# Performance work log

Measured on AMD Instinct MI355X. Metric: run time of the kernel, lower is better.

Reference implementation:

```python
import jax, jax.numpy as jnp
import numpy as np

D = 768
H = 8
HD = D // H
FF = 4 * D


def _linear_params(key, din, dout):
    kw, kb = jax.random.split(key)
    lim = 1.0 / np.sqrt(din)
    W = jax.random.uniform(kw, (din, dout), jnp.float32, -lim, lim)
    b = jax.random.uniform(kb, (dout,), jnp.float32, -lim, lim)
    return W, b


def setup_inputs() -> dict:
    key = jax.random.key(0)
    ks = jax.random.split(key, 8)
    x = jax.random.normal(ks[0], (16, 1024, D), jnp.float32)
    Wq, bq = _linear_params(ks[1], D, D)
    Wk, bk = _linear_params(ks[2], D, D)
    Wv, bv = _linear_params(ks[3], D, D)
    Wo, bo = _linear_params(ks[4], D, D)
    W1, b1 = _linear_params(ks[5], D, FF)
    W2, b2 = _linear_params(ks[6], FF, D)
    gamma = jnp.ones((D,), jnp.float32)
    beta = jnp.zeros((D,), jnp.float32)
    return {"x": x, "gamma": gamma, "beta": beta,
            "Wq": Wq, "bq": bq, "Wk": Wk, "bk": bk, "Wv": Wv, "bv": bv,
            "Wo": Wo, "bo": bo, "W1": W1, "b1": b1, "W2": W2, "b2": b2}


def _layernorm(x, gamma, beta, eps=1e-5):
    mu = jnp.mean(x, axis=-1, keepdims=True)
    var = jnp.var(x, axis=-1, keepdims=True)
    return (x - mu) * jax.lax.rsqrt(var + eps) * gamma + beta


def _block(x, gamma, beta, Wq, bq, Wk, bk, Wv, bv, Wo, bo, W1, b1, W2, b2):
    b, n, d = x.shape
    residual = x
    h = _layernorm(x, gamma, beta)
    # QKV projections -> [b, h, n, hd]
    q = (h @ Wq + bq).reshape(b, n, H, HD).transpose(0, 2, 1, 3)
    k = (h @ Wk + bk).reshape(b, n, H, HD).transpose(0, 2, 1, 3)
    v = (h @ Wv + bv).reshape(b, n, H, HD).transpose(0, 2, 1, 3)
    scale = HD ** 0.5
    scores = jnp.einsum('bhid,bhjd->bhij', q, k) / scale
    attn = jax.nn.softmax(scores, axis=-1)
    out = jnp.einsum('bhij,bhjd->bhid', attn, v)
    out = out.transpose(0, 2, 1, 3).reshape(b, n, d)
    out = out @ Wo + bo
    out = out + residual
    residual = out
    h = _layernorm(out, gamma, beta)  # same LN params reused (as in source)
    h = jax.nn.gelu(h @ W1 + b1, approximate=False)
    h = h @ W2 + b2
    return h + residual


def reference(x, gamma, beta, Wq, bq, Wk, bk, Wv, bv, Wo, bo, W1, b1, W2, b2):
    return _block(x, gamma, beta, Wq, bq, Wk, bk, Wv, bv, Wo, bo, W1, b1, W2, b2)
```

## Files before the change

kernel.cpp:

```cpp
#include <hip/hip_runtime.h>

typedef unsigned short u16;
typedef float f32x4 __attribute__((ext_vector_type(4)));
typedef __bf16 bf16x8 __attribute__((ext_vector_type(8)));

#define AS1 __attribute__((address_space(1)))
#define AS3 __attribute__((address_space(3)))

__device__ __forceinline__ float bf2f(u16 h) {
  return __uint_as_float(((unsigned)h) << 16);
}
__device__ __forceinline__ u16 f2bf(float f) {
  unsigned u = __float_as_uint(f);
  unsigned r = (u + 0x7FFFu + ((u >> 16) & 1u)) >> 16;
  return (u16)r;
}
__device__ __forceinline__ void gload16(const u16* g, u16* l) {
  __builtin_amdgcn_global_load_lds((const AS1 void*)g, (AS3 void*)l, 16, 0, 0);
}

__global__ void transpose_k(const float* __restrict__ in, u16* __restrict__ out,
                            int R, int C) {
  __shared__ u16 t[32][33];
  int c0 = blockIdx.x * 32, r0 = blockIdx.y * 32;
  int tx = threadIdx.x & 31, ty = threadIdx.x >> 5;
  for (int i = 0; i < 32; i += 8)
    t[ty + i][tx] = f2bf(in[(size_t)(r0 + ty + i) * C + c0 + tx]);
  __syncthreads();
  for (int i = 0; i < 32; i += 8)
    out[(size_t)(c0 + ty + i) * R + r0 + tx] = t[tx][ty + i];
}

__global__ void transpose4_k(const float* __restrict__ s0, const float* __restrict__ s1,
                             const float* __restrict__ s2, const float* __restrict__ s3,
                             u16* __restrict__ d0, u16* __restrict__ d1,
                             u16* __restrict__ d2, u16* __restrict__ d3) {
  __shared__ u16 t[32][33];
  const float* in = (blockIdx.z == 0) ? s0 : (blockIdx.z == 1) ? s1
                    : (blockIdx.z == 2) ? s2 : s3;
  u16* out = (blockIdx.z == 0) ? d0 : (blockIdx.z == 1) ? d1
             : (blockIdx.z == 2) ? d2 : d3;
  int c0 = blockIdx.x * 32, r0 = blockIdx.y * 32;
  int tx = threadIdx.x & 31, ty = threadIdx.x >> 5;
  for (int i = 0; i < 32; i += 8)
    t[ty + i][tx] = f2bf(in[(size_t)(r0 + ty + i) * 768 + c0 + tx]);
  __syncthreads();
  for (int i = 0; i < 32; i += 8)
    out[(size_t)(c0 + ty + i) * 768 + r0 + tx] = t[tx][ty + i];
}

__global__ void pack3_k(const float* __restrict__ a, const float* __restrict__ b,
                        const float* __restrict__ c, float* __restrict__ out) {
  int i = blockIdx.x * 256 + threadIdx.x;
  float v = (i < 768) ? a[i] : (i < 1536) ? b[i - 768] : c[i - 1536];
  out[i] = v;
}

#define QLD 2304
__global__ void vtrans_k(const u16* __restrict__ qkv, u16* __restrict__ vt) {
  __shared__ u16 t[32][33];
  int bh = blockIdx.z, b = bh >> 3, h = bh & 7;
  int n0 = blockIdx.y * 32, d0 = blockIdx.x * 32;
  int tx = threadIdx.x & 31, ty = threadIdx.x >> 5;
  const u16* src = qkv + (size_t)(b * 1024) * QLD + 1536 + h * 96;
  for (int i = 0; i < 32; i += 8)
    t[ty + i][tx] = src[(size_t)(n0 + ty + i) * QLD + d0 + tx];
  __syncthreads();
  u16* dst = vt + ((size_t)bh * 96 + d0) * 1024 + n0;
  for (int i = 0; i < 32; i += 8)
    dst[(size_t)(ty + i) * 1024 + tx] = t[tx][ty + i];
}

__global__ __launch_bounds__(256) void ln_f32_k(const float* __restrict__ x,
                                                const float* __restrict__ gamma,
                                                const float* __restrict__ beta,
                                                u16* __restrict__ out) {
  __shared__ float red[8];
  int row = blockIdx.x, t = threadIdx.x;
  const float* xr = x + (size_t)row * 768;
  float v[3], s = 0.f, s2 = 0.f;
#pragma unroll
  for (int i = 0; i < 3; i++) {
    v[i] = xr[t + i * 256];
    s += v[i]; s2 += v[i] * v[i];
  }
#pragma unroll
  for (int off = 1; off < 64; off <<= 1) {
    s += __shfl_xor(s, off, 64);
    s2 += __shfl_xor(s2, off, 64);
  }
  int w = t >> 6;
  if ((t & 63) == 0) { red[w] = s; red[4 + w] = s2; }
  __syncthreads();
  s = red[0] + red[1] + red[2] + red[3];
  s2 = red[4] + red[5] + red[6] + red[7];
  float mu = s * (1.f / 768.f);
  float var = s2 * (1.f / 768.f) - mu * mu;
  float rs = rsqrtf(var + 1e-5f);
  u16* orow = out + (size_t)row * 768;
#pragma unroll
  for (int i = 0; i < 3; i++) {
    int c = t + i * 256;
    orow[c] = f2bf((v[i] - mu) * rs * gamma[c] + beta[c]);
  }
}

#define BM 128
#define BN 128
#define BK 64

template <int EPI>
__global__ __launch_bounds__(256, 4) void gemm_bt(
    const u16* __restrict__ A, const u16* __restrict__ Bt,
    const float* __restrict__ bias, const float* __restrict__ res,
    void* __restrict__ Cv, int M, int N, int K, int lda) {
  __shared__ u16 As[BM * BK];
  __shared__ u16 Bs[BN * BK];
  int tid = threadIdx.x, lane = tid & 63, w = tid >> 6;
  int l15 = lane & 15, quad = lane >> 4;
  int wm = (w >> 1) * 64, wn = (w & 1) * 64;
  int GX = gridDim.x;
  int f = blockIdx.y * GX + blockIdx.x;
  int mpx = GX >> 3;
  int xcd = f & 7, idx = f >> 3;
  int m0 = (xcd * mpx + (idx % mpx)) * BM;
  int n0 = (idx / mpx) * BN;
  int NT = K / BK;
  int sr[4], sc[4];
#pragma unroll
  for (int i = 0; i < 4; i++) {
    int c = w * 4 + i;
    sr[i] = (c >> 1) * 16 + l15;
    sc[i] = (c & 1) * 32 + quad * 8;
  }
  f32x4 acc[4][4] = {};
  for (int t = 0; t < NT; t++) {
    __syncthreads();
    int k0 = t * BK;
#pragma unroll
    for (int i = 0; i < 4; i++) {
      int c = w * 4 + i;
      gload16(A + (size_t)(m0 + sr[i]) * lda + k0 + sc[i], As + c * 512);
      gload16(Bt + (size_t)(n0 + sr[i]) * K + k0 + sc[i], Bs + c * 512);
    }
    __syncthreads();
#pragma unroll
    for (int kk = 0; kk < 2; kk++) {
      bf16x8 af[4], bfv[4];
#pragma unroll
      for (int i = 0; i < 4; i++) {
        int ga = (w >> 1) * 4 + i;
        int gb = (w & 1) * 4 + i;
        af[i] = *(const bf16x8*)(As + (ga * 2 + kk) * 512 + lane * 8);
        bfv[i] = *(const bf16x8*)(Bs + (gb * 2 + kk) * 512 + lane * 8);
      }
#pragma unroll
      for (int mt = 0; mt < 4; mt++)
#pragma unroll
        for (int nt = 0; nt < 4; nt++)
          acc[mt][nt] = __builtin_amdgcn_mfma_f32_16x16x32_bf16(
              af[mt], bfv[nt], acc[mt][nt], 0, 0, 0);
    }
  }
#pragma unroll
  for (int nt = 0; nt < 4; nt++) {
    int col = n0 + wn + nt * 16 + l15;
    float bv = bias[col];
#pragma unroll
    for (int mt = 0; mt < 4; mt++) {
      int row = m0 + wm + mt * 16 + quad * 4;
#pragma unroll
      for (int r = 0; r < 4; r++) {
        float v = acc[mt][nt][r] + bv;
        size_t idx2 = (size_t)(row + r) * N + col;
        if (EPI == 4) {
          v += res[idx2];
          ((float*)Cv)[idx2] = v;
        } else {
          if (EPI == 2) v = 0.5f * v * (1.0f + erff(v * 0.70710678118654752f));
          ((u16*)Cv)[idx2] = f2bf(v);
        }
      }
    }
  }
}

#define QSS 104
#define VSS 72
#define PSS 72
__global__ __launch_bounds__(256, 2) void attn_k(const u16* __restrict__ qkv,
                                                 const u16* __restrict__ vt,
                                                 u16* __restrict__ o) {
  __shared__ u16 qs[64 * QSS];
  __shared__ u16 ks[2][64 * QSS];
  __shared__ u16 vts[2][96 * VSS];
  __shared__ u16 ps[4 * 16 * PSS];
  int tid = threadIdx.x, lane = tid & 63, w = tid >> 6;
  int l15 = lane & 15, quad = lane >> 4;
  int f = blockIdx.y * 16 + blockIdx.x;
  int xcd = f & 7, idx = f >> 3;
  int bh = xcd * 16 + (idx & 15);
  int qt = idx >> 4;
  int b = bh >> 3, h = bh & 7;
  const u16* qbase = qkv + (size_t)(b * 1024 + qt * 64) * QLD + h * 96;
  const u16* kbase = qkv + (size_t)(b * 1024) * QLD + 768 + h * 96;
  const u16* vtbase = vt + (size_t)bh * 96 * 1024;
  int kr[3], ko[3], vr[3], vo[3];
#pragma unroll
  for (int i = 0; i < 3; i++) {
    int c = tid + i * 256;
    kr[i] = c / 12; ko[i] = (c % 12) * 8;
    vr[i] = c >> 3; vo[i] = (c & 7) * 8;
  }
#pragma unroll
  for (int i = 0; i < 3; i++)
    *(uint4*)(qs + kr[i] * QSS + ko[i]) =
        *(const uint4*)(qbase + (size_t)kr[i] * QLD + ko[i]);
  uint4 kreg[3], vreg[3];
#pragma unroll
  for (int i = 0; i < 3; i++) {
    kreg[i] = *(const uint4*)(kbase + (size_t)kr[i] * QLD + ko[i]);
    vreg[i] = *(const uint4*)(vtbase + (size_t)vr[i] * 1024 + vo[i]);
  }
#pragma unroll
  for (int i = 0; i < 3; i++) {
    *(uint4*)(ks[0] + kr[i] * QSS + ko[i]) = kreg[i];
    *(uint4*)(vts[0] + vr[i] * VSS + vo[i]) = vreg[i];
  }
  __syncthreads();

  float mi[4], li[4];
#pragma unroll
  for (int r = 0; r < 4; r++) { mi[r] = -1e30f; li[r] = 0.f; }
  f32x4 oacc[6] = {};
  const float scale = 0.10206207261596577f;
  for (int kt = 0; kt < 16; kt++) {
    int cur = kt & 1, nxt = cur ^ 1;
    int ktn = (kt + 1) & 15;
#pragma unroll
    for (int i = 0; i < 3; i++) {
      kreg[i] = *(const uint4*)(kbase + (size_t)(ktn * 64 + kr[i]) * QLD + ko[i]);
      vreg[i] = *(const uint4*)(vtbase + (size_t)vr[i] * 1024 + ktn * 64 + vo[i]);
    }
    f32x4 s[4] = {};
#pragma unroll
    for (int kk = 0; kk < 3; kk++) {
      bf16x8 a = *(const bf16x8*)(qs + (w * 16 + l15) * QSS + kk * 32 + quad * 8);
#pragma unroll
      for (int nt = 0; nt < 4; nt++) {
        bf16x8 bb =
            *(const bf16x8*)(ks[cur] + (nt * 16 + l15) * QSS + kk * 32 + quad * 8);
        s[nt] = __builtin_amdgcn_mfma_f32_16x16x32_bf16(a, bb, s[nt], 0, 0, 0);
      }
    }
#pragma unroll
    for (int r = 0; r < 4; r++) {
      float sv[4], mx = -1e30f;
#pragma unroll
      for (int nt = 0; nt < 4; nt++) {
        sv[nt] = s[nt][r];
        mx = fmaxf(mx, sv[nt]);
      }
#pragma unroll
      for (int off = 1; off < 16; off <<= 1) mx = fmaxf(mx, __shfl_xor(mx, off, 16));
      float mnew = fmaxf(mi[r], mx);
      float alpha = __expf((mi[r] - mnew) * scale);
      float rs = 0.f;
#pragma unroll
      for (int nt = 0; nt < 4; nt++) {
        sv[nt] = __expf((sv[nt] - mnew) * scale);
        rs += sv[nt];
      }
      li[r] = li[r] * alpha + rs;
      mi[r] = mnew;
#pragma unroll
      for (int ht = 0; ht < 6; ht++) oacc[ht][r] *= alpha;
      int prow = quad * 4 + r;
#pragma unroll
      for (int nt = 0; nt < 4; nt++)
        ps[w * 16 * PSS + prow * PSS + nt * 16 + l15] = f2bf(sv[nt]);
    }
    asm volatile("s_waitcnt lgkmcnt(0)" ::: "memory");
#pragma unroll
    for (int kk = 0; kk < 2; kk++) {
      bf16x8 a = *(const bf16x8*)(ps + w * 16 * PSS + l15 * PSS + kk * 32 + quad * 8);
#pragma unroll
      for (int ht = 0; ht < 6; ht++) {
        bf16x8 bb =
            *(const bf16x8*)(vts[cur] + (ht * 16 + l15) * VSS + kk * 32 + quad * 8);
        oacc[ht] = __builtin_amdgcn_mfma_f32_16x16x32_bf16(a, bb, oacc[ht], 0, 0, 0);
      }
    }
#pragma unroll
    for (int i = 0; i < 3; i++) {
      *(uint4*)(ks[nxt] + kr[i] * QSS + ko[i]) = kreg[i];
      *(uint4*)(vts[nxt] + vr[i] * VSS + vo[i]) = vreg[i];
    }
    __syncthreads();
  }
#pragma unroll
  for (int r = 0; r < 4; r++)
#pragma unroll
    for (int off = 1; off < 16; off <<= 1) li[r] += __shfl_xor(li[r], off, 16);
  u16* obase = o + (size_t)(b * 1024 + qt * 64 + w * 16) * 768 + h * 96;
#pragma unroll
  for (int r = 0; r < 4; r++) {
    float inv = 1.0f / li[r];
    int row = quad * 4 + r;
#pragma unroll
    for (int ht = 0; ht < 6; ht++)
      obase[(size_t)row * 768 + ht * 16 + l15] = f2bf(oacc[ht][r] * inv);
  }
}

extern "C" void kernel_launch(void* const* d_in, const int* in_sizes, int n_in,
                              void* d_out, int out_size, void* d_ws,
                              size_t ws_size, hipStream_t stream) {
  const float* x = (const float*)d_in[0];
  const float* gamma = (const float*)d_in[1];
  const float* beta = (const float*)d_in[2];
  const float* Wq = (const float*)d_in[3];
  const float* bq = (const float*)d_in[4];
  const float* Wk = (const float*)d_in[5];
  const float* bk = (const float*)d_in[6];
  const float* Wv = (const float*)d_in[7];
  const float* bv = (const float*)d_in[8];
  const float* Wo = (const float*)d_in[9];
  const float* bo = (const float*)d_in[10];
  const float* W1 = (const float*)d_in[11];
  const float* b1 = (const float*)d_in[12];
  const float* W2 = (const float*)d_in[13];
  const float* b2 = (const float*)d_in[14];
  float* out = (float*)d_out;

  char* ws = (char*)d_ws;
  size_t off = 0;
  auto alloc = [&](size_t elems) {
    u16* p = (u16*)(ws + off);
    off += elems * sizeof(u16);
    return p;
  };
  u16* WqT = alloc(768 * 768);
  u16* WkT = alloc(768 * 768);
  u16* WvT = alloc(768 * 768);
  u16* WoT = alloc(768 * 768);
  u16* W1T = alloc((size_t)768 * 3072);
  u16* W2T = alloc((size_t)3072 * 768);
  float* bqkv = (float*)(ws + off); off += 2304 * sizeof(float);
  u16* hb = alloc((size_t)16384 * 768);
  u16* qkvb = alloc((size_t)16384 * 2304);
  u16* vtb = (u16*)d_out;

  transpose4_k<<<dim3(24, 24, 4), 256, 0, stream>>>(Wq, Wk, Wv, Wo,
                                                    WqT, WkT, WvT, WoT);
  transpose_k<<<dim3(96, 24), 256, 0, stream>>>(W1, W1T, 768, 3072);
  transpose_k<<<dim3(24, 96), 256, 0, stream>>>(W2, W2T, 3072, 768);
  pack3_k<<<9, 256, 0, stream>>>(bq, bk, bv, bqkv);

  ln_f32_k<<<16384, 256, 0, stream>>>(x, gamma, beta, hb);
  gemm_bt<0><<<dim3(128, 18), 256, 0, stream>>>(hb, WqT, bqkv, nullptr, qkvb,
                                                16384, 2304, 768, 768);
  vtrans_k<<<dim3(3, 32, 128), 256, 0, stream>>>(qkvb, vtb);
  attn_k<<<dim3(16, 128), 256, 0, stream>>>(qkvb, vtb, hb);
  gemm_bt<4><<<dim3(128, 6), 256, 0, stream>>>(hb, WoT, bo, x, out,
                                               16384, 768, 768, 768);
  ln_f32_k<<<16384, 256, 0, stream>>>(out, gamma, beta, hb);
  for (int c = 0; c < 2; c++) {
    const u16* h2c = hb + (size_t)c * 8192 * 768;
    const float* y1c = out + (size_t)c * 8192 * 768;
    float* outc = out + (size_t)c * 8192 * 768;
    gemm_bt<2><<<dim3(64, 24), 256, 0, stream>>>(h2c, W1T, b1, nullptr, qkvb,
                                                 8192, 3072, 768, 768);
    gemm_bt<4><<<dim3(64, 6), 256, 0, stream>>>(qkvb, W2T, b2, y1c, outc,
                                                8192, 768, 3072, 3072);
  }
}
```

Before: 838.0 us.

## Add 512-thread 256x64-tile GEMM and split QKV output into separate buffers

```diff
diff --git a/kernel.cpp b/kernel.cpp
--- a/kernel.cpp
+++ b/kernel.cpp
@@ -56,15 +56,14 @@
   out[i] = v;
 }
 
-#define QLD 2304
-__global__ void vtrans_k(const u16* __restrict__ qkv, u16* __restrict__ vt) {
+__global__ void vtrans_k(const u16* __restrict__ v, u16* __restrict__ vt) {
   __shared__ u16 t[32][33];
   int bh = blockIdx.z, b = bh >> 3, h = bh & 7;
   int n0 = blockIdx.y * 32, d0 = blockIdx.x * 32;
   int tx = threadIdx.x & 31, ty = threadIdx.x >> 5;
-  const u16* src = qkv + (size_t)(b * 1024) * QLD + 1536 + h * 96;
-  for (int i = 0; i < 32; i += 8)
-    t[ty + i][tx] = src[(size_t)(n0 + ty + i) * QLD + d0 + tx];
+  const u16* src = v + (size_t)(b * 1024) * 768 + h * 96;
+  for (int i = 0; i < 32; i += 8)
+    t[ty + i][tx] = src[(size_t)(n0 + ty + i) * 768 + d0 + tx];
   __syncthreads();
   u16* dst = vt + ((size_t)bh * 96 + d0) * 1024 + n0;
   for (int i = 0; i < 32; i += 8)
@@ -185,10 +184,104 @@
   }
 }
 
+template <int EPI>
+__global__ __launch_bounds__(512, 4) void gemm512_bt(
+    const u16* __restrict__ A, const u16* __restrict__ Bt,
+    const float* __restrict__ bias, const float* __restrict__ res,
+    void* __restrict__ Cv, int M, int N, int K, int lda) {
+  __shared__ u16 As[2][256 * 64];
+  __shared__ u16 Bs[2][64 * 64];
+  int tid = threadIdx.x, lane = tid & 63, w = tid >> 6;
+  int l15 = lane & 15, quad = lane >> 4;
+  int wr = w >> 1, wc = w & 1;
+  int GX = gridDim.x;
+  int f = blockIdx.y * GX + blockIdx.x;
+  int mpx = GX >> 3;
+  int xcd = f & 7, idx = f >> 3;
+  int m0 = (xcd * mpx + (idx % mpx)) * 256;
+  int n0 = (idx / mpx) * 64;
+  int NT = K / 64;
+#pragma unroll
+  for (int i = 0; i < 4; i++) {
+    int c = w * 4 + i;
+    gload16(A + (size_t)(m0 + (c >> 1) * 16 + l15) * lda + (c & 1) * 32 + quad * 8,
+            As[0] + c * 512);
+  }
+  gload16(Bt + (size_t)(n0 + (w >> 1) * 16 + l15) * K + (w & 1) * 32 + quad * 8,
+          Bs[0] + w * 512);
+  f32x4 acc[4][2] = {};
+  for (int t = 0; t < NT; t++) {
+    int cur = t & 1;
+    int k0 = (t + 1 < NT) ? (t + 1) * 64 : 0;
+#pragma unroll
+    for (int i = 0; i < 4; i++) {
+      int c = w * 4 + i;
+      gload16(A + (size_t)(m0 + (c >> 1) * 16 + l15) * lda + k0 + (c & 1) * 32 + quad * 8,
+              As[cur ^ 1] + c * 512);
+    }
+    gload16(Bt + (size_t)(n0 + (w >> 1) * 16 + l15) * K + k0 + (w & 1) * 32 + quad * 8,
+            Bs[cur ^ 1] + w * 512);
+    asm volatile("s_waitcnt vmcnt(5)" ::: "memory");
+    __builtin_amdgcn_s_barrier();
+    const u16* ab = As[cur];
+    const u16* bb = Bs[cur];
+#pragma unroll
+    for (int kk = 0; kk < 2; kk++) {
+      bf16x8 af[4], bfv[2];
+#pragma unroll
+      for (int i = 0; i < 4; i++) {
+        int rg = wr * 4 + i;
+        af[i] = *(const bf16x8*)(ab + (rg * 2 + kk) * 512 + lane * 8);
+      }
+#pragma unroll
+      for (int i = 0; i < 2; i++) {
+        int rg = wc * 2 + i;
+        bfv[i] = *(const bf16x8*)(bb + (rg * 2 + kk) * 512 + lane * 8);
+      }
+#pragma unroll
+      for (int mt = 0; mt < 4; mt++)
+#pragma unroll
+        for (int nt = 0; nt < 2; nt++)
+          acc[mt][nt] = __builtin_amdgcn_mfma_f32_16x16x32_bf16(
+              af[mt], bfv[nt], acc[mt][nt], 0, 0, 0);
+    }
+    __builtin_amdgcn_s_barrier();
+  }
+  asm volatile("s_waitcnt vmcnt(0)" ::: "memory");
+  int seg = (EPI == 1) ? (n0 >= 1536 ? 2 : (n0 >= 768 ? 1 : 0)) : 0;
+#pragma unroll
+  for (int nt = 0; nt < 2; nt++) {
+    int col = n0 + wc * 32 + nt * 16 + l15;
+    float bv = bias[col];
+#pragma unroll
+    for (int mt = 0; mt < 4; mt++) {
+      int row = m0 + wr * 64 + mt * 16 + quad * 4;
+#pragma unroll
+      for (int r = 0; r < 4; r++) {
+        float v = acc[mt][nt][r] + bv;
+        if (EPI == 1) {
+          u16* outp = (u16*)Cv + (size_t)seg * 16384 * 768;
+          outp[(size_t)(row + r) * 768 + (col - seg * 768)] = f2bf(v);
+        } else {
+          size_t idx2 = (size_t)(row + r) * N + col;
+          if (EPI == 4) {
+            v += res[idx2];
+            ((float*)Cv)[idx2] = v;
+          } else {
+            if (EPI == 2) v = 0.5f * v * (1.0f + erff(v * 0.70710678118654752f));
+            ((u16*)Cv)[idx2] = f2bf(v);
+          }
+        }
+      }
+    }
+  }
+}
+
 #define QSS 104
 #define VSS 72
 #define PSS 72
-__global__ __launch_bounds__(256, 2) void attn_k(const u16* __restrict__ qkv,
+__global__ __launch_bounds__(256, 2) void attn_k(const u16* __restrict__ q,
+                                                 const u16* __restrict__ k,
                                                  const u16* __restrict__ vt,
                                                  u16* __restrict__ o) {
   __shared__ u16 qs[64 * QSS];
@@ -202,8 +295,8 @@
   int bh = xcd * 16 + (idx & 15);
   int qt = idx >> 4;
   int b = bh >> 3, h = bh & 7;
-  const u16* qbase = qkv + (size_t)(b * 1024 + qt * 64) * QLD + h * 96;
-  const u16* kbase = qkv + (size_t)(b * 1024) * QLD + 768 + h * 96;
+  const u16* qbase = q + (size_t)(b * 1024 + qt * 64) * 768 + h * 96;
+  const u16* kbase = k + (size_t)(b * 1024) * 768 + h * 96;
   const u16* vtbase = vt + (size_t)bh * 96 * 1024;
   int kr[3], ko[3], vr[3], vo[3];
 #pragma unroll
@@ -215,11 +308,11 @@
 #pragma unroll
   for (int i = 0; i < 3; i++)
     *(uint4*)(qs + kr[i] * QSS + ko[i]) =
-        *(const uint4*)(qbase + (size_t)kr[i] * QLD + ko[i]);
+        *(const uint4*)(qbase + (size_t)kr[i] * 768 + ko[i]);
   uint4 kreg[3], vreg[3];
 #pragma unroll
   for (int i = 0; i < 3; i++) {
-    kreg[i] = *(const uint4*)(kbase + (size_t)kr[i] * QLD + ko[i]);
+    kreg[i] = *(const uint4*)(kbase + (size_t)kr[i] * 768 + ko[i]);
     vreg[i] = *(const uint4*)(vtbase + (size_t)vr[i] * 1024 + vo[i]);
   }
 #pragma unroll
@@ -239,7 +332,7 @@
     int ktn = (kt + 1) & 15;
 #pragma unroll
     for (int i = 0; i < 3; i++) {
-      kreg[i] = *(const uint4*)(kbase + (size_t)(ktn * 64 + kr[i]) * QLD + ko[i]);
+      kreg[i] = *(const uint4*)(kbase + (size_t)(ktn * 64 + kr[i]) * 768 + ko[i]);
       vreg[i] = *(const uint4*)(vtbase + (size_t)vr[i] * 1024 + ktn * 64 + vo[i]);
     }
     f32x4 s[4] = {};
@@ -348,7 +441,9 @@
   u16* W2T = alloc((size_t)3072 * 768);
   float* bqkv = (float*)(ws + off); off += 2304 * sizeof(float);
   u16* hb = alloc((size_t)16384 * 768);
-  u16* qkvb = alloc((size_t)16384 * 2304);
+  u16* qb = alloc((size_t)16384 * 768);
+  u16* kb = alloc((size_t)16384 * 768);
+  u16* vb = alloc((size_t)16384 * 768);
   u16* vtb = (u16*)d_out;
 
   transpose4_k<<<dim3(24, 24, 4), 256, 0, stream>>>(Wq, Wk, Wv, Wo,
@@ -358,20 +453,21 @@
   pack3_k<<<9, 256, 0, stream>>>(bq, bk, bv, bqkv);
 
   ln_f32_k<<<16384, 256, 0, stream>>>(x, gamma, beta, hb);
-  gemm_bt<0><<<dim3(128, 18), 256, 0, stream>>>(hb, WqT, bqkv, nullptr, qkvb,
-                                                16384, 2304, 768, 768);
-  vtrans_k<<<dim3(3, 32, 128), 256, 0, stream>>>(qkvb, vtb);
-  attn_k<<<dim3(16, 128), 256, 0, stream>>>(qkvb, vtb, hb);
-  gemm_bt<4><<<dim3(128, 6), 256, 0, stream>>>(hb, WoT, bo, x, out,
-                                               16384, 768, 768, 768);
-  ln_f32_k<<<16384, 256, 0, stream>>>(out, gamma, beta, hb);
+  gemm512_bt<1><<<dim3(64, 36), 512, 0, stream>>>(hb, WqT, bqkv, nullptr, qb,
+                                                  16384, 2304, 768, 768);
+  vtrans_k<<<dim3(3, 32, 128), 256, 0, stream>>>(vb, vtb);
+  attn_k<<<dim3(16, 128), 256, 0, stream>>>(qb, kb, vtb, vb);
+  gemm512_bt<4><<<dim3(64, 12), 512, 0, stream>>>(vb, WoT, bo, x, out,
+                                                  16384, 768, 768, 768);
+  ln_f32_k<<<16384, 256, 0, stream>>>(out, gamma, beta, kb);
+  u16* fbuf = hb;
   for (int c = 0; c < 2; c++) {
-    const u16* h2c = hb + (size_t)c * 8192 * 768;
+    const u16* h2c = kb + (size_t)c * 8192 * 768;
     const float* y1c = out + (size_t)c * 8192 * 768;
     float* outc = out + (size_t)c * 8192 * 768;
-    gemm_bt<2><<<dim3(64, 24), 256, 0, stream>>>(h2c, W1T, b1, nullptr, qkvb,
-                                                 8192, 3072, 768, 768);
-    gemm_bt<4><<<dim3(64, 6), 256, 0, stream>>>(qkvb, W2T, b2, y1c, outc,
+    gemm512_bt<2><<<dim3(32, 48), 512, 0, stream>>>(h2c, W1T, b1, nullptr,
+                                                    fbuf, 8192, 3072, 768, 768);
+    gemm_bt<4><<<dim3(64, 6), 256, 0, stream>>>(fbuf, W2T, b2, y1c, outc,
                                                 8192, 768, 3072, 3072);
   }
 }
```

New measurement: 931.3 us. +11.1%, slower.
